# Kernel tuning notes

Hardware: AMD Instinct MI355X
Metric: run time of the kernel (lower is better)

## Reference

```python
import jax, jax.numpy as jnp
import numpy as np

N, F_IN, F_OUT, HEADS = 4096, 128, 64, 4


def setup_inputs() -> dict:
    key = jax.random.key(0)
    k1, k2, k3, k4, k5 = jax.random.split(key, 5)
    X = jax.random.normal(k1, (N, F_IN), dtype=jnp.float32)
    A = jax.random.randint(k2, (N, N), 0, 2, dtype=jnp.int32)
    # zero the diagonal: the torch loop always prepends the self node, so the
    # adjacency must not also contain it (would duplicate the self term).
    A = A * (1 - jnp.eye(N, dtype=jnp.int32))
    # per-head Linear(F_IN, F_OUT) weights/bias and Linear(2*F_OUT, 1, bias=False)
    W = jax.random.normal(k3, (HEADS, F_OUT, F_IN), dtype=jnp.float32) / np.sqrt(F_IN)
    b = jax.random.normal(k4, (HEADS, F_OUT), dtype=jnp.float32) * 0.02
    att = jax.random.normal(k5, (HEADS, 2 * F_OUT), dtype=jnp.float32) / np.sqrt(2 * F_OUT)
    return {"X": X, "A": A, "W": W, "b": b, "att": att}


def reference(X, A, W, b, att):
    # H[h, n, o] = line_h(X)
    H = jnp.einsum('nf,hof->hno', X, W) + b[:, None, :]
    f_out = W.shape[1]
    a_src, a_dst = att[:, :f_out], att[:, f_out:]
    # score e_ij = leaky_relu(a_src.H_i + a_dst.H_j)
    s = jnp.einsum('hno,ho->hn', H, a_src)  # query-side term (xi_bar expanded)
    d = jnp.einsum('hno,ho->hn', H, a_dst)  # neighbor-side term
    e = jax.nn.leaky_relu(s[:, :, None] + d[:, None, :])  # [H, N, N]
    # neighbor set = {self} U {j : A_ij != 0}
    mask = (A > 0) | jnp.eye(A.shape[0], dtype=bool)
    e = jnp.where(mask[None], e, -jnp.inf)
    alpha = jax.nn.softmax(e, axis=-1)  # segment softmax per node row
    # weighted sum per head, then mean over heads (sum / head in the original)
    out = jnp.einsum('hnm,hmo->no', alpha, H) / W.shape[0]
    return out  # [N, F_OUT]
```

## Files before the change

### kernel.cpp

```cpp
#include <hip/hip_runtime.h>
#include <hip/hip_bf16.h>


#define NN 4096
#define FIN 128
#define FOUT 64
#define NH 4

typedef __attribute__((ext_vector_type(8))) short bf16x8;
typedef __attribute__((ext_vector_type(4))) float f32x4;
typedef __attribute__((ext_vector_type(4))) unsigned int u32x4;

__device__ __forceinline__ unsigned short f32_bf16(float f) {
    unsigned u = __builtin_bit_cast(unsigned, f);
    u += 0x7fffu + ((u >> 16) & 1u);
    return (unsigned short)(u >> 16);
}

__global__ __launch_bounds__(256) void pack_bits(
    const int* __restrict__ A, unsigned long long* __restrict__ Abits)
{
    const int row  = blockIdx.x;
    const int lane = threadIdx.x & 63;
    const int wv   = threadIdx.x >> 6;
    const int* arow = A + (size_t)row * NN;
    #pragma unroll 4
    for (int c = 0; c < 16; ++c) {
        const int col = c * 256 + wv * 64 + lane;
        unsigned long long m = __ballot(__builtin_nontemporal_load(&arow[col]) > 0);
        if (lane == 0) Abits[(size_t)row * 64 + c * 4 + wv] = m;
    }
}

__global__ __launch_bounds__(256) void gat_prep(
    const float* __restrict__ X, const float* __restrict__ W,
    const float* __restrict__ b, const float* __restrict__ att,
    unsigned short* __restrict__ HbfT, float* __restrict__ Hrow,
    float* __restrict__ s_out, float* __restrict__ d_out,
    float* __restrict__ es_g, float* __restrict__ es2_g,
    float* __restrict__ ed_g, float* __restrict__ ed2_g)
{
    const int rb = blockIdx.x;
    const int h  = blockIdx.y;
    const int n0 = rb * 32;
    const int t  = threadIdx.x;

    __shared__ float Xl[32][132];
    __shared__ float Wt[128][68];

    for (int g = t; g < 32 * 32; g += 256) {
        int row = g >> 5, c4 = g & 31;
        float4 v = *(const float4*)&X[(size_t)(n0 + row) * FIN + c4 * 4];
        *(float4*)&Xl[row][c4 * 4] = v;
    }
    for (int g = t; g < 64 * 32; g += 256) {
        int o = g >> 5, c4 = g & 31;
        float4 v = *(const float4*)&W[((size_t)h * FOUT + o) * FIN + c4 * 4];
        Wt[c4 * 4 + 0][o] = v.x; Wt[c4 * 4 + 1][o] = v.y;
        Wt[c4 * 4 + 2][o] = v.z; Wt[c4 * 4 + 3][o] = v.w;
    }
    __syncthreads();

    const int rg = t >> 4;
    const int og = t & 15;
    float acc[2][4] = {};

    #pragma unroll 4
    for (int f4 = 0; f4 < 32; ++f4) {
        float xv[2][4], wv[4][4];
        #pragma unroll
        for (int i = 0; i < 2; ++i) {
            float4 tmp = *(const float4*)&Xl[rg * 2 + i][f4 * 4];
            xv[i][0] = tmp.x; xv[i][1] = tmp.y; xv[i][2] = tmp.z; xv[i][3] = tmp.w;
        }
        #pragma unroll
        for (int k = 0; k < 4; ++k) {
            float4 tmp = *(const float4*)&Wt[f4 * 4 + k][og * 4];
            wv[k][0] = tmp.x; wv[k][1] = tmp.y; wv[k][2] = tmp.z; wv[k][3] = tmp.w;
        }
        #pragma unroll
        for (int i = 0; i < 2; ++i)
            #pragma unroll
            for (int k = 0; k < 4; ++k)
                #pragma unroll
                for (int jj = 0; jj < 4; ++jj)
                    acc[i][jj] = fmaf(xv[i][k], wv[k][jj], acc[i][jj]);
    }

    float bb[4], as_[4], ad_[4];
    #pragma unroll
    for (int jj = 0; jj < 4; ++jj) {
        bb[jj]  = b[h * FOUT + og * 4 + jj];
        as_[jj] = att[h * 2 * FOUT + og * 4 + jj];
        ad_[jj] = att[h * 2 * FOUT + FOUT + og * 4 + jj];
    }
    #pragma unroll
    for (int i = 0; i < 2; ++i)
        #pragma unroll
        for (int jj = 0; jj < 4; ++jj)
            acc[i][jj] += bb[jj];

    float sp[2] = {0.f, 0.f}, dp[2] = {0.f, 0.f};
    #pragma unroll
    for (int i = 0; i < 2; ++i)
        #pragma unroll
        for (int jj = 0; jj < 4; ++jj) {
            sp[i] = fmaf(acc[i][jj], as_[jj], sp[i]);
            dp[i] = fmaf(acc[i][jj], ad_[jj], dp[i]);
        }
    #pragma unroll
    for (int off = 1; off < 16; off <<= 1) {
        #pragma unroll
        for (int i = 0; i < 2; ++i) {
            sp[i] += __shfl_xor(sp[i], off);
            dp[i] += __shfl_xor(dp[i], off);
        }
    }
    if (og == 0) {
        #pragma unroll
        for (int i = 0; i < 2; ++i) {
            int nn = n0 + rg * 2 + i;
            s_out[h * NN + nn]  = sp[i];
            d_out[h * NN + nn]  = dp[i];
            es_g [h * NN + nn]  = __expf(sp[i]);
            es2_g[h * NN + nn]  = __expf(0.01f * sp[i]);
            ed_g [h * NN + nn]  = __expf(dp[i]);
            ed2_g[h * NN + nn]  = __expf(0.01f * dp[i]);
        }
    }

    #pragma unroll
    for (int i = 0; i < 2; ++i) {
        float4 v = make_float4(acc[i][0], acc[i][1], acc[i][2], acc[i][3]);
        *(float4*)&Hrow[((size_t)h * NN + n0 + rg * 2 + i) * FOUT + og * 4] = v;
    }
    #pragma unroll
    for (int jj = 0; jj < 4; ++jj) {
        int o = og * 4 + jj;
        ushort2 p;
        p.x = f32_bf16(acc[0][jj]);
        p.y = f32_bf16(acc[1][jj]);
        *(ushort2*)&HbfT[((size_t)h * FOUT + o) * NN + n0 + rg * 2] = p;
    }
}

__global__ __launch_bounds__(512, 8) void gat_main(
    const unsigned* __restrict__ Abits, const unsigned short* __restrict__ HbfT,
    const float* __restrict__ es_g, const float* __restrict__ es2_g,
    const float* __restrict__ ed_g, const float* __restrict__ ed2_g,
    float* __restrict__ Hpart, float* __restrict__ lpartP)
{
    const int id  = blockIdx.x;
    const int grp = id & 31;
    const int h   = grp >> 3;
    const int cg  = grp & 7;
    const int bx  = id >> 5;
    const int n0  = bx * 128;
    const int tid  = threadIdx.x;
    const int w    = tid >> 6;
    const int lane = tid & 63;
    const int r    = lane & 15;
    const int q    = lane >> 4;
    const int qs   = q * 8;

    __shared__ unsigned short Hlds[64][128];
    __shared__ unsigned bits_lds[128 * 5];

    const int n = n0 + w * 16 + r;
    const float es  = es_g [h * NN + n];
    const float es2 = es2_g[h * NN + n];
    const int bits_base = (w * 16 + r) * 5;

    bf16x8 ones;
    #pragma unroll
    for (int i = 0; i < 8; ++i) ones[i] = (short)0x3F80;

    f32x4 acc0 = {0,0,0,0}, acc1 = {0,0,0,0}, acc2 = {0,0,0,0},
          acc3 = {0,0,0,0}, accl = {0,0,0,0};

    for (int ch = 0; ch < 4; ++ch) {
        const int c0 = cg * 512 + ch * 128;
        __syncthreads();

        #pragma unroll
        for (int it = 0; it < 2; ++it) {
            int flat = it * 512 + tid;
            int o    = flat >> 4;
            int c16  = flat & 15;
            int blk  = c16 ^ (o & 15);
            *(bf16x8*)&Hlds[o][blk * 8] =
                *(const bf16x8*)&HbfT[((size_t)h * FOUT + o) * NN + c0 + c16 * 8];
        }
        {
            int row = tid >> 2, wd = tid & 3;
            bits_lds[row * 5 + wd] = Abits[(size_t)(n0 + row) * 128 + (c0 >> 5) + wd];
        }
        __syncthreads();

        const float* edh  = ed_g  + h * NN + c0;
        const float* ed2h = ed2_g + h * NN + c0;

        #pragma unroll
        for (int step = 0; step < 4; ++step) {
            const unsigned bits8 = bits_lds[bits_base + step] >> qs;
            const int mk = step * 32 + qs;

            const float4 e0 = *(const float4*)&edh [mk];
            const float4 e1 = *(const float4*)&edh [mk + 4];
            const float4 g0 = *(const float4*)&ed2h[mk];
            const float4 g1 = *(const float4*)&ed2h[mk + 4];
            const float edv [8] = {e0.x, e0.y, e0.z, e0.w, e1.x, e1.y, e1.z, e1.w};
            const float ed2v[8] = {g0.x, g0.y, g0.z, g0.w, g1.x, g1.y, g1.z, g1.w};

            u32x4 afu;
            #pragma unroll
            for (int p = 0; p < 4; ++p) {
                const int j0 = 2 * p, j1 = 2 * p + 1;
                float wa = (bits8 & (1u << j0))
                         ? fmaxf(es * edv[j0], es2 * ed2v[j0]) : 0.0f;
                float wb = (bits8 & (1u << j1))
                         ? fmaxf(es * edv[j1], es2 * ed2v[j1]) : 0.0f;
                __hip_bfloat162 pk = __float22bfloat162_rn(make_float2(wa, wb));
                unsigned u;
                __builtin_memcpy(&u, &pk, sizeof(u));
                afu[p] = u;
            }
            const bf16x8 af = __builtin_bit_cast(bf16x8, afu);

            const int mb = (step * 4 + q) ^ r;
            const bf16x8 b0 = *(const bf16x8*)&Hlds[r     ][mb * 8];
            const bf16x8 b1 = *(const bf16x8*)&Hlds[r + 16][mb * 8];
            const bf16x8 b2 = *(const bf16x8*)&Hlds[r + 32][mb * 8];
            const bf16x8 b3 = *(const bf16x8*)&Hlds[r + 48][mb * 8];

            acc0 = __builtin_amdgcn_mfma_f32_16x16x32_bf16(af, b0,   acc0, 0, 0, 0);
            acc1 = __builtin_amdgcn_mfma_f32_16x16x32_bf16(af, b1,   acc1, 0, 0, 0);
            acc2 = __builtin_amdgcn_mfma_f32_16x16x32_bf16(af, b2,   acc2, 0, 0, 0);
            acc3 = __builtin_amdgcn_mfma_f32_16x16x32_bf16(af, b3,   acc3, 0, 0, 0);
            accl = __builtin_amdgcn_mfma_f32_16x16x32_bf16(af, ones, accl, 0, 0, 0);
        }
    }

    float* hb = Hpart + ((size_t)(cg * NH + h) * NN + n0 + w * 16) * FOUT;
    #pragma unroll
    for (int reg = 0; reg < 4; ++reg) {
        const int rr = q * 4 + reg;
        hb[rr * FOUT +  0 + r] = acc0[reg];
        hb[rr * FOUT + 16 + r] = acc1[reg];
        hb[rr * FOUT + 32 + r] = acc2[reg];
        hb[rr * FOUT + 48 + r] = acc3[reg];
    }
    if (r == 0) {
        #pragma unroll
        for (int reg = 0; reg < 4; ++reg)
            lpartP[(size_t)(cg * NH + h) * NN + n0 + w * 16 + q * 4 + reg] = accl[reg];
    }
}

__global__ __launch_bounds__(256) void gat_fin(
    const float* __restrict__ Hpart, const float* __restrict__ Hrow,
    const float* __restrict__ lpartP, const float* __restrict__ s_g,
    const float* __restrict__ d_g, float* __restrict__ out)
{
    const int tid = threadIdx.x;
    const int rr  = tid >> 4;
    const int c4  = tid & 15;
    const int n   = blockIdx.x * 16 + rr;
    const int o   = c4 * 4;

    float4 res = make_float4(0.f, 0.f, 0.f, 0.f);
    #pragma unroll
    for (int h = 0; h < NH; ++h) {
        float l = 0.f;
        #pragma unroll
        for (int cg = 0; cg < 8; ++cg)
            l += lpartP[(size_t)(cg * NH + h) * NN + n];
        float tt = s_g[h * NN + n] + d_g[h * NN + n];
        float wd = __expf(fmaxf(tt, 0.01f * tt));
        float inv = 0.25f / (l + wd);

        f32x4 ha = {0.f, 0.f, 0.f, 0.f};
        #pragma unroll
        for (int cg = 0; cg < 8; ++cg) {
            f32x4 hp = __builtin_nontemporal_load(
                (const f32x4*)&Hpart[((size_t)(cg * NH + h) * NN + n) * FOUT + o]);
            ha += hp;
        }
        float4 hr = *(const float4*)&Hrow[((size_t)h * NN + n) * FOUT + o];

        res.x += (ha[0] + wd * hr.x) * inv;
        res.y += (ha[1] + wd * hr.y) * inv;
        res.z += (ha[2] + wd * hr.z) * inv;
        res.w += (ha[3] + wd * hr.w) * inv;
    }
    *(float4*)&out[(size_t)n * FOUT + o] = res;
}

extern "C" void kernel_launch(void* const* d_in, const int* in_sizes, int n_in,
                              void* d_out, int out_size, void* d_ws, size_t ws_size,
                              hipStream_t stream) {
    const float* X   = (const float*)d_in[0];
    const int*   A   = (const int*)  d_in[1];
    const float* W   = (const float*)d_in[2];
    const float* b   = (const float*)d_in[3];
    const float* att = (const float*)d_in[4];
    float* out = (float*)d_out;

    char* ws = (char*)d_ws;
    unsigned short* HbfT = (unsigned short*)ws;
    size_t off = (size_t)NH * FOUT * NN * 2;
    float* s_buf   = (float*)(ws + off);  off += (size_t)NH * NN * 4;
    float* d_buf   = (float*)(ws + off);  off += (size_t)NH * NN * 4;
    float* es_buf  = (float*)(ws + off);  off += (size_t)NH * NN * 4;
    float* es2_buf = (float*)(ws + off);  off += (size_t)NH * NN * 4;
    float* ed_buf  = (float*)(ws + off);  off += (size_t)NH * NN * 4;
    float* ed2_buf = (float*)(ws + off);  off += (size_t)NH * NN * 4;
    unsigned long long* Abits = (unsigned long long*)(ws + off);
    off += (size_t)NN * 64 * 8;
    float* Hrow   = (float*)(ws + off);
    off += (size_t)NH * NN * FOUT * 4;
    float* Hpart  = (float*)(ws + off);
    off += (size_t)8 * NH * NN * FOUT * 4;
    float* lpartP = (float*)(ws + off);
    off += (size_t)8 * NH * NN * 4;

    pack_bits<<<NN, 256, 0, stream>>>(A, Abits);
    gat_prep<<<dim3(128, 4), 256, 0, stream>>>(X, W, b, att, HbfT, Hrow,
                                               s_buf, d_buf,
                                               es_buf, es2_buf, ed_buf, ed2_buf);
    gat_main<<<1024, 512, 0, stream>>>((const unsigned*)Abits, HbfT,
                                       es_buf, es2_buf, ed_buf, ed2_buf,
                                       Hpart, lpartP);
    gat_fin<<<256, 256, 0, stream>>>(Hpart, Hrow, lpartP, s_buf, d_buf, out);
}
```

Measured before the change: 168.4 us.

## Merge bit-packing into prep kernel and double main-loop column chunk

Folds the adjacency bit-packing kernel into the projection prep kernel as extra blocks of one launch, removing a launch and letting both phases run concurrently. In the main attention kernel, each block now stages 256 columns of H and adjacency bits per chunk instead of 128, halving the number of barrier-separated chunk iterations. The LDS swizzle is widened to 32 blocks to match. LDS use per block doubles, which may reduce occupancy.

```diff
diff --git a/kernel.cpp b/kernel.cpp
--- a/kernel.cpp
+++ b/kernel.cpp
@@ -17,36 +17,39 @@
     return (unsigned short)(u >> 16);
 }
 
-__global__ __launch_bounds__(256) void pack_bits(
-    const int* __restrict__ A, unsigned long long* __restrict__ Abits)
-{
-    const int row  = blockIdx.x;
-    const int lane = threadIdx.x & 63;
-    const int wv   = threadIdx.x >> 6;
-    const int* arow = A + (size_t)row * NN;
-    #pragma unroll 4
-    for (int c = 0; c < 16; ++c) {
-        const int col = c * 256 + wv * 64 + lane;
-        unsigned long long m = __ballot(__builtin_nontemporal_load(&arow[col]) > 0);
-        if (lane == 0) Abits[(size_t)row * 64 + c * 4 + wv] = m;
-    }
-}
-
-__global__ __launch_bounds__(256) void gat_prep(
+__global__ __launch_bounds__(256) void gat_pp(
     const float* __restrict__ X, const float* __restrict__ W,
     const float* __restrict__ b, const float* __restrict__ att,
+    const int* __restrict__ A, unsigned long long* __restrict__ Abits,
     unsigned short* __restrict__ HbfT, float* __restrict__ Hrow,
     float* __restrict__ s_out, float* __restrict__ d_out,
     float* __restrict__ es_g, float* __restrict__ es2_g,
     float* __restrict__ ed_g, float* __restrict__ ed2_g)
 {
-    const int rb = blockIdx.x;
-    const int h  = blockIdx.y;
-    const int n0 = rb * 32;
-    const int t  = threadIdx.x;
-
     __shared__ float Xl[32][132];
     __shared__ float Wt[128][68];
+
+    const int bid = blockIdx.x;
+    const int t   = threadIdx.x;
+
+    if (bid >= 512) {
+        const int row  = bid - 512;
+        const int lane = t & 63;
+        const int wv   = t >> 6;
+        const int* arow = A + (size_t)row * NN;
+        #pragma unroll 4
+        for (int c = 0; c < 16; ++c) {
+            const int col = c * 256 + wv * 64 + lane;
+            unsigned long long m =
+                __ballot(__builtin_nontemporal_load(&arow[col]) > 0);
+            if (lane == 0) Abits[(size_t)row * 64 + c * 4 + wv] = m;
+        }
+        return;
+    }
+
+    const int rb = bid & 127;
+    const int h  = bid >> 7;
+    const int n0 = rb * 32;
 
     for (int g = t; g < 32 * 32; g += 256) {
         int row = g >> 5, c4 = g & 31;
@@ -163,13 +166,13 @@
     const int q    = lane >> 4;
     const int qs   = q * 8;
 
-    __shared__ unsigned short Hlds[64][128];
-    __shared__ unsigned bits_lds[128 * 5];
+    __shared__ unsigned short Hlds[64][256];
+    __shared__ unsigned bits_lds[128 * 9];
 
     const int n = n0 + w * 16 + r;
     const float es  = es_g [h * NN + n];
     const float es2 = es2_g[h * NN + n];
-    const int bits_base = (w * 16 + r) * 5;
+    const int bits_base = (w * 16 + r) * 9;
 
     bf16x8 ones;
     #pragma unroll
@@ -178,22 +181,26 @@
     f32x4 acc0 = {0,0,0,0}, acc1 = {0,0,0,0}, acc2 = {0,0,0,0},
           acc3 = {0,0,0,0}, accl = {0,0,0,0};
 
-    for (int ch = 0; ch < 4; ++ch) {
-        const int c0 = cg * 512 + ch * 128;
+    const unsigned short* hbase = HbfT + (size_t)h * FOUT * NN;
+
+    for (int ch = 0; ch < 2; ++ch) {
+        const int c0 = cg * 512 + ch * 256;
         __syncthreads();
 
+        #pragma unroll
+        for (int it = 0; it < 4; ++it) {
+            int flat = it * 512 + tid;
+            int o    = flat >> 5;
+            int c16  = flat & 31;
+            int blk  = c16 ^ (o & 31);
+            *(bf16x8*)&Hlds[o][blk * 8] =
+                *(const bf16x8*)&hbase[(size_t)o * NN + c0 + c16 * 8];
+        }
         #pragma unroll
         for (int it = 0; it < 2; ++it) {
             int flat = it * 512 + tid;
-            int o    = flat >> 4;
-            int c16  = flat & 15;
-            int blk  = c16 ^ (o & 15);
-            *(bf16x8*)&Hlds[o][blk * 8] =
-                *(const bf16x8*)&HbfT[((size_t)h * FOUT + o) * NN + c0 + c16 * 8];
-        }
-        {
-            int row = tid >> 2, wd = tid & 3;
-            bits_lds[row * 5 + wd] = Abits[(size_t)(n0 + row) * 128 + (c0 >> 5) + wd];
+            int row = flat >> 3, wd = flat & 7;
+            bits_lds[row * 9 + wd] = Abits[(size_t)(n0 + row) * 128 + (c0 >> 5) + wd];
         }
         __syncthreads();
 
@@ -201,7 +208,7 @@
         const float* ed2h = ed2_g + h * NN + c0;
 
         #pragma unroll
-        for (int step = 0; step < 4; ++step) {
+        for (int step = 0; step < 8; ++step) {
             const unsigned bits8 = bits_lds[bits_base + step] >> qs;
             const int mk = step * 32 + qs;
 
@@ -227,11 +234,13 @@
             }
             const bf16x8 af = __builtin_bit_cast(bf16x8, afu);
 
-            const int mb = (step * 4 + q) ^ r;
-            const bf16x8 b0 = *(const bf16x8*)&Hlds[r     ][mb * 8];
-            const bf16x8 b1 = *(const bf16x8*)&Hlds[r + 16][mb * 8];
-            const bf16x8 b2 = *(const bf16x8*)&Hlds[r + 32][mb * 8];
-            const bf16x8 b3 = *(const bf16x8*)&Hlds[r + 48][mb * 8];
+            const int mb   = step * 4 + q;
+            const int mbx0 = mb ^ r;
+            const int mbx1 = mb ^ (r + 16);
+            const bf16x8 b0 = *(const bf16x8*)&Hlds[r     ][mbx0 * 8];
+            const bf16x8 b1 = *(const bf16x8*)&Hlds[r + 16][mbx1 * 8];
+            const bf16x8 b2 = *(const bf16x8*)&Hlds[r + 32][mbx0 * 8];
+            const bf16x8 b3 = *(const bf16x8*)&Hlds[r + 48][mbx1 * 8];
 
             acc0 = __builtin_amdgcn_mfma_f32_16x16x32_bf16(af, b0,   acc0, 0, 0, 0);
             acc1 = __builtin_amdgcn_mfma_f32_16x16x32_bf16(af, b1,   acc1, 0, 0, 0);
@@ -324,10 +333,9 @@
     float* lpartP = (float*)(ws + off);
     off += (size_t)8 * NH * NN * 4;
 
-    pack_bits<<<NN, 256, 0, stream>>>(A, Abits);
-    gat_prep<<<dim3(128, 4), 256, 0, stream>>>(X, W, b, att, HbfT, Hrow,
-                                               s_buf, d_buf,
-                                               es_buf, es2_buf, ed_buf, ed2_buf);
+    gat_pp<<<512 + NN, 256, 0, stream>>>(X, W, b, att, A, Abits, HbfT, Hrow,
+                                         s_buf, d_buf,
+                                         es_buf, es2_buf, ed_buf, ed2_buf);
     gat_main<<<1024, 512, 0, stream>>>((const unsigned*)Abits, HbfT,
                                        es_buf, es2_buf, ed_buf, ed2_buf,
                                        Hpart, lpartP);
```

Result: slower. 210.5 us (+25.1%).
